# Kernel optimization log

Measured on AMD Instinct MI355X. Metric: run time of the kernel, lower is better.

Reference implementation:

```python
import jax, jax.numpy as jnp
import numpy as np

B, S, IX, OX, H = 4, 2048, 1024, 1024, 16
DH = OX // H  # head dim = 64


def setup_inputs() -> dict:
    key = jax.random.key(0)
    k1, k2, k3, k4, k5 = jax.random.split(key, 5)
    x = jax.random.normal(k1, (B, S, IX), dtype=jnp.float32)
    w1 = jax.random.normal(k2, (IX, 3 * OX), dtype=jnp.float32) * 0.02
    b1 = jnp.zeros((1, 3 * OX), dtype=jnp.float32)
    w2 = jax.random.normal(k3, (OX, IX), dtype=jnp.float32) * 0.02
    b2 = jnp.zeros((1, IX), dtype=jnp.float32)
    return {"x": x, "w1": w1, "b1": b1, "w2": w2, "b2": b2}


def _attention(x, w1, b1, w2, b2):
    # fused QKV projection: (B,S,IX) @ (IX,3*OX)
    qkv = jnp.einsum('bsi,io->bso', x, w1) + b1  # (B,S,3*OX)
    k, q, v = jnp.split(qkv, 3, axis=-1)  # NOTE original split order is k,q,v
    # split heads: (B,S,OX) -> (B,H,S,DH)
    def split_heads(t):
        return t.reshape(B, S, H, DH).transpose(0, 2, 1, 3)
    k, q, v = split_heads(k), split_heads(q), split_heads(v)
    # original code calls sdpa(k, q, v): scores = K @ Q^T / sqrt(DH)
    scores = jnp.einsum('bhsd,bhtd->bhst', k, q) / jnp.sqrt(jnp.float32(DH))
    attn = jax.nn.softmax(scores, axis=-1)  # (B,H,S,S)
    out = jnp.einsum('bhst,bhtd->bhsd', attn, v)  # (B,H,S,DH)
    # merge heads -> (B,S,OX)
    out = out.transpose(0, 2, 1, 3).reshape(B, S, OX)
    # output projection OX -> IX
    return jnp.einsum('bso,oi->bsi', out, w2) + b2


def reference(x, w1, b1, w2, b2):
    return _attention(x, w1, b1, w2, b2)
```

## Files before the change

### kernel.cpp

```cpp
#include <hip/hip_runtime.h>
#include <hip/hip_bf16.h>
#include <stdint.h>

#define B_   4
#define S_   2048
#define IX_  1024
#define OX_  1024
#define H_   16
#define DH_  64
#define MROWS (B_*S_)
#define NQKV  (3*OX_)

typedef __bf16 bf16x8 __attribute__((ext_vector_type(8)));
typedef float  f32x4  __attribute__((ext_vector_type(4)));

typedef __attribute__((address_space(1))) const uint8_t* gp_t;
typedef __attribute__((address_space(3))) uint8_t*       sp_t;

__device__ __forceinline__ void load_lds16(const void* g, void* s) {
  __builtin_amdgcn_global_load_lds((gp_t)g, (sp_t)s, 16, 0, 0);
}

__device__ __forceinline__ ushort f2bf(float f) {
  union { float f; uint32_t u; } x; x.f = f;
  uint32_t lsb = (x.u >> 16) & 1u;
  x.u += 0x7fffu + lsb;
  return (ushort)(x.u >> 16);
}

__global__ void cvt_bf16(const float* __restrict__ in, ushort* __restrict__ out, int n4) {
  int i = blockIdx.x * blockDim.x + threadIdx.x;
  if (i < n4) {
    float4 v = ((const float4*)in)[i];
    ushort4 o;
    o.x = f2bf(v.x); o.y = f2bf(v.y); o.z = f2bf(v.z); o.w = f2bf(v.w);
    ((ushort4*)out)[i] = o;
  }
}

__global__ void transpose_cvt(const float* __restrict__ in, ushort* __restrict__ out,
                              int K, int N) {
  __shared__ float tile[32][33];
  int n0 = blockIdx.x * 32, k0 = blockIdx.y * 32;
  int tx = threadIdx.x, ty = threadIdx.y;
  #pragma unroll
  for (int j = ty; j < 32; j += 8)
    tile[j][tx] = in[(size_t)(k0 + j) * N + n0 + tx];
  __syncthreads();
  #pragma unroll
  for (int j = ty; j < 32; j += 8)
    out[(size_t)(n0 + j) * K + k0 + tx] = f2bf(tile[tx][j]);
}

template<int OUTF32>
__global__ __launch_bounds__(256, 2) void gemm_bt(
    const ushort* __restrict__ A, const ushort* __restrict__ Bt,
    const float* __restrict__ bias, void* __restrict__ Cv,
    int M, int N, int K)
{
  __shared__ alignas(16) ushort As[128 * 32];
  __shared__ alignas(16) ushort Bs[128 * 32];
  const int t = threadIdx.x;
  const int wave = t >> 6, lane = t & 63;
  const int wr = wave >> 1, wc = wave & 1;
  const int lr = lane & 15, lk = (lane >> 4) * 8;
  const int brow = blockIdx.x * 128, bcol = blockIdx.y * 128;

  f32x4 acc[4][4] = {};

  for (int k0 = 0; k0 < K; k0 += 32) {
    #pragma unroll
    for (int i = 0; i < 2; ++i) {
      int chunk = wave * 128 + i * 64 + lane;
      int row = chunk >> 2, c8 = (chunk & 3) * 8;
      load_lds16(A  + (size_t)(brow + row) * K + k0 + c8, &As[(wave * 128 + i * 64) * 8]);
      load_lds16(Bt + (size_t)(bcol + row) * K + k0 + c8, &Bs[(wave * 128 + i * 64) * 8]);
    }
    __syncthreads();
    bf16x8 af[4], bfr[4];
    #pragma unroll
    for (int mi = 0; mi < 4; ++mi)
      af[mi] = *(const bf16x8*)&As[(wr * 64 + mi * 16 + lr) * 32 + lk];
    #pragma unroll
    for (int ni = 0; ni < 4; ++ni)
      bfr[ni] = *(const bf16x8*)&Bs[(wc * 64 + ni * 16 + lr) * 32 + lk];
    #pragma unroll
    for (int mi = 0; mi < 4; ++mi)
      #pragma unroll
      for (int ni = 0; ni < 4; ++ni)
        acc[mi][ni] = __builtin_amdgcn_mfma_f32_16x16x32_bf16(af[mi], bfr[ni], acc[mi][ni], 0, 0, 0);
    __syncthreads();
  }

  #pragma unroll
  for (int mi = 0; mi < 4; ++mi) {
    #pragma unroll
    for (int ni = 0; ni < 4; ++ni) {
      int col = bcol + wc * 64 + ni * 16 + lr;
      float bv = bias[col];
      #pragma unroll
      for (int j = 0; j < 4; ++j) {
        int row = brow + wr * 64 + mi * 16 + (lane >> 4) * 4 + j;
        float v = acc[mi][ni][j] + bv;
        if (OUTF32) ((float*)Cv)[(size_t)row * N + col] = v;
        else        ((ushort*)Cv)[(size_t)row * N + col] = f2bf(v);
      }
    }
  }
}

__global__ __launch_bounds__(256, 3) void flash_attn(
    const ushort* __restrict__ qkv, ushort* __restrict__ out)
{
  __shared__ alignas(16) ushort Ks[2][64 * 64];
  __shared__ alignas(16) ushort Vs[2][64 * 64];
  __shared__ alignas(16) ushort Ps[128 * 64];

  const int t = threadIdx.x;
  const int wave = t >> 6, lane = t & 63;
  const int lr = lane & 15, lg = lane >> 4;
  const int bx = blockIdx.x;
  const int bh = blockIdx.y;
  const int b = bh >> 4, h = bh & 15;

  const size_t base = (size_t)b * S_ * NQKV;
  const ushort* Kg = qkv + base + h * DH_;
  const ushort* Qg = qkv + base + OX_ + h * DH_;
  const ushort* Vg = qkv + base + 2 * OX_ + h * DH_;
  const int s0 = bx * 128;

  const int vt0 = (t >> 3) * 2;
  const int vd8 = (t & 7) * 8;

  #pragma unroll
  for (int i = 0; i < 2; ++i) {
    int chunk = i * 256 + t;
    int row = chunk >> 3;
    int cg = (chunk & 7) ^ (row & 7);
    load_lds16(Qg + (size_t)row * NQKV + cg * 8, &Ks[0][chunk * 8]);
  }
  uint4 v0 = *(const uint4*)(Vg + (size_t)vt0 * NQKV + vd8);
  uint4 v1 = *(const uint4*)(Vg + (size_t)(vt0 + 1) * NQKV + vd8);
  #pragma unroll
  for (int i = 0; i < 4; ++i) {
    int chunk = wave * 256 + i * 64 + lane;
    int row = chunk >> 3;
    int cg = (chunk & 7) ^ (row & 7);
    load_lds16(Kg + (size_t)(s0 + row) * NQKV + cg * 8, &Ps[chunk * 8]);
  }
  __syncthreads();

  bf16x8 aq[2][2];
  #pragma unroll
  for (int mi = 0; mi < 2; ++mi)
    #pragma unroll
    for (int kk = 0; kk < 2; ++kk) {
      int r = wave * 32 + mi * 16 + lr;
      aq[mi][kk] = *(const bf16x8*)&Ps[r * 64 + (((kk * 4 + lg) ^ (r & 7)) * 8)];
    }

  {
    #pragma unroll
    for (int j = 0; j < 8; ++j) {
      uint32_t a = ((const uint32_t*)&v0)[j >> 1];
      uint32_t bb = ((const uint32_t*)&v1)[j >> 1];
      uint32_t lo = (j & 1) ? (a >> 16) : (a & 0xffffu);
      uint32_t hi = (j & 1) ? (bb >> 16) : (bb & 0xffffu);
      int d = vd8 + j;
      int ch = (vt0 >> 3) ^ ((d ^ (d >> 3)) & 7);
      *(uint32_t*)((uint8_t*)&Vs[0][0] + d * 128 + ch * 16 + ((vt0 >> 1) & 3) * 4)
          = lo | (hi << 16);
    }
  }
  __syncthreads();

  f32x4 oacc[2][4] = {};
  float lrun[2][4] = {};

  for (int kt = 0; kt < 32; ++kt) {
    const int cur = kt & 1;
    const int t0n = (kt + 1) * 64;
    uint4 v0n, v1n;
    if (kt < 31) {
      #pragma unroll
      for (int i = 0; i < 2; ++i) {
        int chunk = i * 256 + t;
        int row = chunk >> 3;
        int cg = (chunk & 7) ^ (row & 7);
        load_lds16(Qg + (size_t)(t0n + row) * NQKV + cg * 8, &Ks[cur ^ 1][chunk * 8]);
      }
      v0n = *(const uint4*)(Vg + (size_t)(t0n + vt0) * NQKV + vd8);
      v1n = *(const uint4*)(Vg + (size_t)(t0n + vt0 + 1) * NQKV + vd8);
    }

    f32x4 sacc[2][4] = {};
    #pragma unroll
    for (int kk = 0; kk < 2; ++kk) {
      #pragma unroll
      for (int ni = 0; ni < 4; ++ni) {
        int rk = ni * 16 + lr;
        bf16x8 bk = *(const bf16x8*)&Ks[cur][rk * 64 + (((kk * 4 + lg) ^ (rk & 7)) * 8)];
        #pragma unroll
        for (int mi = 0; mi < 2; ++mi)
          sacc[mi][ni] = __builtin_amdgcn_mfma_f32_16x16x32_bf16(aq[mi][kk], bk, sacc[mi][ni], 0, 0, 0);
      }
    }

    #pragma unroll
    for (int mi = 0; mi < 2; ++mi) {
      #pragma unroll
      for (int j = 0; j < 4; ++j) {
        int prow = wave * 32 + mi * 16 + lg * 4 + j;
        float rs = 0.f;
        #pragma unroll
        for (int ni = 0; ni < 4; ++ni) {
          float p = __expf(sacc[mi][ni][j] * 0.125f);
          rs += p;
          int pchunk = (ni * 2 + (lr >> 3)) ^ (prow & 7);
          Ps[prow * 64 + pchunk * 8 + (lr & 7)] = f2bf(p);
        }
        lrun[mi][j] += rs;
      }
    }

    #pragma unroll
    for (int kk = 0; kk < 2; ++kk) {
      bf16x8 ap[2];
      #pragma unroll
      for (int mi = 0; mi < 2; ++mi) {
        int prow = wave * 32 + mi * 16 + lr;
        ap[mi] = *(const bf16x8*)&Ps[prow * 64 + (((kk * 4 + lg) ^ (prow & 7)) * 8)];
      }
      #pragma unroll
      for (int nd = 0; nd < 4; ++nd) {
        int dr = nd * 16 + lr;
        int ch = (kk * 4 + lg) ^ ((dr ^ (dr >> 3)) & 7);
        bf16x8 bv = *(const bf16x8*)&Vs[cur][dr * 64 + ch * 8];
        #pragma unroll
        for (int mi = 0; mi < 2; ++mi)
          oacc[mi][nd] = __builtin_amdgcn_mfma_f32_16x16x32_bf16(ap[mi], bv, oacc[mi][nd], 0, 0, 0);
      }
    }

    if (kt < 31) {
      #pragma unroll
      for (int j = 0; j < 8; ++j) {
        uint32_t a = ((const uint32_t*)&v0n)[j >> 1];
        uint32_t bb = ((const uint32_t*)&v1n)[j >> 1];
        uint32_t lo = (j & 1) ? (a >> 16) : (a & 0xffffu);
        uint32_t hi = (j & 1) ? (bb >> 16) : (bb & 0xffffu);
        int d = vd8 + j;
        int ch = (vt0 >> 3) ^ ((d ^ (d >> 3)) & 7);
        *(uint32_t*)((uint8_t*)&Vs[cur ^ 1][0] + d * 128 + ch * 16 + ((vt0 >> 1) & 3) * 4)
            = lo | (hi << 16);
      }
    }
    __syncthreads();
  }

  #pragma unroll
  for (int mi = 0; mi < 2; ++mi)
    #pragma unroll
    for (int j = 0; j < 4; ++j) {
      float s = lrun[mi][j];
      #pragma unroll
      for (int m = 1; m < 16; m <<= 1) s += __shfl_xor(s, m, 64);
      lrun[mi][j] = s;
    }

  #pragma unroll
  for (int mi = 0; mi < 2; ++mi) {
    #pragma unroll
    for (int nd = 0; nd < 4; ++nd) {
      int d = nd * 16 + lr;
      #pragma unroll
      for (int j = 0; j < 4; ++j) {
        int row = s0 + wave * 32 + mi * 16 + lg * 4 + j;
        float v = oacc[mi][nd][j] / lrun[mi][j];
        out[(size_t)(b * S_ + row) * OX_ + h * DH_ + d] = f2bf(v);
      }
    }
  }
}

extern "C" void kernel_launch(void* const* d_in, const int* in_sizes, int n_in,
                              void* d_out, int out_size, void* d_ws, size_t ws_size,
                              hipStream_t stream) {
  const float* x  = (const float*)d_in[0];
  const float* w1 = (const float*)d_in[1];
  const float* b1 = (const float*)d_in[2];
  const float* w2 = (const float*)d_in[3];
  const float* b2 = (const float*)d_in[4];
  float* out = (float*)d_out;
  uint8_t* ws = (uint8_t*)d_ws;

  ushort* xb   = (ushort*)(ws);
  ushort* w1t  = (ushort*)(ws + 16777216);
  ushort* w2t  = (ushort*)(ws + 23068672);
  ushort* qkv  = (ushort*)(ws + 25165824);
  ushort* attn = (ushort*)(ws + 75497472);

  hipLaunchKernelGGL(cvt_bf16, dim3(8192), dim3(256), 0, stream, x, xb, MROWS * IX_ / 4);
  hipLaunchKernelGGL(transpose_cvt, dim3(NQKV / 32, IX_ / 32), dim3(32, 8), 0, stream,
                     w1, w1t, IX_, NQKV);
  hipLaunchKernelGGL(transpose_cvt, dim3(IX_ / 32, OX_ / 32), dim3(32, 8), 0, stream,
                     w2, w2t, OX_, IX_);
  hipLaunchKernelGGL((gemm_bt<0>), dim3(MROWS / 128, NQKV / 128), dim3(256), 0, stream,
                     xb, w1t, b1, (void*)qkv, MROWS, NQKV, IX_);
  hipLaunchKernelGGL(flash_attn, dim3(S_ / 128, B_ * H_), dim3(256), 0, stream, qkv, attn);
  hipLaunchKernelGGL((gemm_bt<1>), dim3(MROWS / 128, IX_ / 128), dim3(256), 0, stream,
                     attn, w2t, b2, (void*)out, MROWS, IX_, OX_);
}
```

Measured before the change: 319.3 us.

## Compute transposed attention tiles so softmax rows land per-lane with packed bf16 stores

Swaps the MFMA operand order in both attention matmuls so the score and output accumulators are transposed, putting each query row in one lane's registers. This lets the exp/sum and the bf16 conversion use packed v_cvt_pk_bf16 with 8-byte LDS and global stores, and cuts the row-sum reduction to two shuffles. It also raises wave priority around the MFMA blocks with s_setprio. The cost is a different LDS write pattern for P, which might bring bank conflicts, and hardware rounding replaces the software f2bf.

```diff
diff --git a/kernel.cpp b/kernel.cpp
--- a/kernel.cpp
+++ b/kernel.cpp
@@ -26,6 +26,12 @@
   uint32_t lsb = (x.u >> 16) & 1u;
   x.u += 0x7fffu + lsb;
   return (ushort)(x.u >> 16);
+}
+
+__device__ __forceinline__ uint32_t cvt_pk_bf16(float lo, float hi) {
+  uint32_t r;
+  asm("v_cvt_pk_bf16_f32 %0, %1, %2" : "=v"(r) : "v"(lo), "v"(hi));
+  return r;
 }
 
 __global__ void cvt_bf16(const float* __restrict__ in, ushort* __restrict__ out, int n4) {
@@ -152,11 +158,11 @@
 
   bf16x8 aq[2][2];
   #pragma unroll
-  for (int mi = 0; mi < 2; ++mi)
+  for (int si = 0; si < 2; ++si)
     #pragma unroll
     for (int kk = 0; kk < 2; ++kk) {
-      int r = wave * 32 + mi * 16 + lr;
-      aq[mi][kk] = *(const bf16x8*)&Ps[r * 64 + (((kk * 4 + lg) ^ (r & 7)) * 8)];
+      int r = wave * 32 + si * 16 + lr;
+      aq[si][kk] = *(const bf16x8*)&Ps[r * 64 + (((kk * 4 + lg) ^ (r & 7)) * 8)];
     }
 
   {
@@ -174,8 +180,8 @@
   }
   __syncthreads();
 
-  f32x4 oacc[2][4] = {};
-  float lrun[2][4] = {};
+  f32x4 oT[4][2] = {};
+  float lrun[2] = {};
 
   for (int kt = 0; kt < 32; ++kt) {
     const int cur = kt & 1;
@@ -193,54 +199,60 @@
       v1n = *(const uint4*)(Vg + (size_t)(t0n + vt0 + 1) * NQKV + vd8);
     }
 
-    f32x4 sacc[2][4] = {};
+    f32x4 sT[4][2] = {};
+    __builtin_amdgcn_s_setprio(1);
     #pragma unroll
     for (int kk = 0; kk < 2; ++kk) {
       #pragma unroll
-      for (int ni = 0; ni < 4; ++ni) {
-        int rk = ni * 16 + lr;
-        bf16x8 bk = *(const bf16x8*)&Ks[cur][rk * 64 + (((kk * 4 + lg) ^ (rk & 7)) * 8)];
+      for (int ti = 0; ti < 4; ++ti) {
+        int rt = ti * 16 + lr;
+        bf16x8 ak = *(const bf16x8*)&Ks[cur][rt * 64 + (((kk * 4 + lg) ^ (rt & 7)) * 8)];
         #pragma unroll
-        for (int mi = 0; mi < 2; ++mi)
-          sacc[mi][ni] = __builtin_amdgcn_mfma_f32_16x16x32_bf16(aq[mi][kk], bk, sacc[mi][ni], 0, 0, 0);
-      }
-    }
-
-    #pragma unroll
-    for (int mi = 0; mi < 2; ++mi) {
-      #pragma unroll
-      for (int j = 0; j < 4; ++j) {
-        int prow = wave * 32 + mi * 16 + lg * 4 + j;
-        float rs = 0.f;
-        #pragma unroll
-        for (int ni = 0; ni < 4; ++ni) {
-          float p = __expf(sacc[mi][ni][j] * 0.125f);
-          rs += p;
-          int pchunk = (ni * 2 + (lr >> 3)) ^ (prow & 7);
-          Ps[prow * 64 + pchunk * 8 + (lr & 7)] = f2bf(p);
-        }
-        lrun[mi][j] += rs;
-      }
-    }
-
+        for (int si = 0; si < 2; ++si)
+          sT[ti][si] = __builtin_amdgcn_mfma_f32_16x16x32_bf16(ak, aq[si][kk], sT[ti][si], 0, 0, 0);
+      }
+    }
+    __builtin_amdgcn_s_setprio(0);
+
+    #pragma unroll
+    for (int si = 0; si < 2; ++si) {
+      int s_loc = wave * 32 + si * 16 + lr;
+      int sx = s_loc & 7;
+      #pragma unroll
+      for (int ti = 0; ti < 4; ++ti) {
+        float p0 = __expf(sT[ti][si][0] * 0.125f);
+        float p1 = __expf(sT[ti][si][1] * 0.125f);
+        float p2 = __expf(sT[ti][si][2] * 0.125f);
+        float p3 = __expf(sT[ti][si][3] * 0.125f);
+        lrun[si] += (p0 + p1) + (p2 + p3);
+        uint32_t u0 = cvt_pk_bf16(p0, p1);
+        uint32_t u1 = cvt_pk_bf16(p2, p3);
+        int p = ti * 8 + lg * 2;
+        uint8_t* dst = (uint8_t*)Ps + s_loc * 128 + (((p >> 2) ^ sx) * 16) + (p & 3) * 4;
+        *(uint2*)dst = make_uint2(u0, u1);
+      }
+    }
+
+    __builtin_amdgcn_s_setprio(1);
     #pragma unroll
     for (int kk = 0; kk < 2; ++kk) {
-      bf16x8 ap[2];
-      #pragma unroll
-      for (int mi = 0; mi < 2; ++mi) {
-        int prow = wave * 32 + mi * 16 + lr;
-        ap[mi] = *(const bf16x8*)&Ps[prow * 64 + (((kk * 4 + lg) ^ (prow & 7)) * 8)];
+      bf16x8 bp[2];
+      #pragma unroll
+      for (int si = 0; si < 2; ++si) {
+        int s_loc = wave * 32 + si * 16 + lr;
+        bp[si] = *(const bf16x8*)&Ps[s_loc * 64 + (((kk * 4 + lg) ^ (s_loc & 7)) * 8)];
       }
       #pragma unroll
       for (int nd = 0; nd < 4; ++nd) {
         int dr = nd * 16 + lr;
         int ch = (kk * 4 + lg) ^ ((dr ^ (dr >> 3)) & 7);
-        bf16x8 bv = *(const bf16x8*)&Vs[cur][dr * 64 + ch * 8];
+        bf16x8 av = *(const bf16x8*)&Vs[cur][dr * 64 + ch * 8];
         #pragma unroll
-        for (int mi = 0; mi < 2; ++mi)
-          oacc[mi][nd] = __builtin_amdgcn_mfma_f32_16x16x32_bf16(ap[mi], bv, oacc[mi][nd], 0, 0, 0);
-      }
-    }
+        for (int si = 0; si < 2; ++si)
+          oT[nd][si] = __builtin_amdgcn_mfma_f32_16x16x32_bf16(av, bp[si], oT[nd][si], 0, 0, 0);
+      }
+    }
+    __builtin_amdgcn_s_setprio(0);
 
     if (kt < 31) {
       #pragma unroll
@@ -258,27 +270,28 @@
     __syncthreads();
   }
 
-  #pragma unroll
-  for (int mi = 0; mi < 2; ++mi)
-    #pragma unroll
-    for (int j = 0; j < 4; ++j) {
-      float s = lrun[mi][j];
-      #pragma unroll
-      for (int m = 1; m < 16; m <<= 1) s += __shfl_xor(s, m, 64);
-      lrun[mi][j] = s;
-    }
-
-  #pragma unroll
-  for (int mi = 0; mi < 2; ++mi) {
-    #pragma unroll
-    for (int nd = 0; nd < 4; ++nd) {
-      int d = nd * 16 + lr;
-      #pragma unroll
-      for (int j = 0; j < 4; ++j) {
-        int row = s0 + wave * 32 + mi * 16 + lg * 4 + j;
-        float v = oacc[mi][nd][j] / lrun[mi][j];
-        out[(size_t)(b * S_ + row) * OX_ + h * DH_ + d] = f2bf(v);
-      }
+  float linv[2];
+  #pragma unroll
+  for (int si = 0; si < 2; ++si) {
+    float s = lrun[si];
+    s += __shfl_xor(s, 16, 64);
+    s += __shfl_xor(s, 32, 64);
+    linv[si] = 1.0f / s;
+  }
+
+  #pragma unroll
+  for (int nd = 0; nd < 4; ++nd) {
+    #pragma unroll
+    for (int si = 0; si < 2; ++si) {
+      float w0 = oT[nd][si][0] * linv[si];
+      float w1 = oT[nd][si][1] * linv[si];
+      float w2 = oT[nd][si][2] * linv[si];
+      float w3 = oT[nd][si][3] * linv[si];
+      uint32_t u0 = cvt_pk_bf16(w0, w1);
+      uint32_t u1 = cvt_pk_bf16(w2, w3);
+      int row = s0 + wave * 32 + si * 16 + lr;
+      int col = h * DH_ + nd * 16 + lg * 4;
+      *(uint2*)&out[(size_t)(b * S_ + row) * OX_ + col] = make_uint2(u0, u1);
     }
   }
 }
```

After: 301.4 us. 5.6% less time.
